# Kernel optimization log

Measured on AMD Instinct MI355X. Metric: run time of the kernel, lower is better.

The kernel has to match this reference:

```python
import jax, jax.numpy as jnp
import numpy as np

HEAD_DIM = 128
B, S = 8, 2048
NEG = -1e9  # matches torch masked_fill value


def setup_inputs() -> dict:
    key = jax.random.key(0)
    kq, kk, kv, kl = jax.random.split(key, 4)
    q = jax.random.normal(kq, (B, S, HEAD_DIM), dtype=jnp.float32)
    k = jax.random.normal(kk, (B, S, HEAD_DIM), dtype=jnp.float32)
    v = jax.random.normal(kv, (B, S, HEAD_DIM), dtype=jnp.float32)
    event_lengths = jax.random.randint(kl, (B,), 0, S, dtype=jnp.int32)
    return {"q": q, "k": k, "v": v, "event_lengths": event_lengths}


def reference(q, k, v, event_lengths):
    # NOTE: the torch module defines query/key/value Linear layers but never
    # applies them in forward(); q, k, v are used raw. Dropout is also unused.
    head_dim = q.shape[-1]
    seq_q = q.shape[1]
    seq_kv = k.shape[1]
    # [B, Sq, Skv] scores
    scores = jnp.einsum("bqd,bkd->bqk", q, k) / jnp.sqrt(
        jnp.asarray(head_dim, dtype=jnp.float32)
    )
    lens = event_lengths[:, None, None]  # [B,1,1]
    mask_q = jnp.arange(seq_q)[None, :, None] < lens   # [B,Sq,1]
    mask_kv = jnp.arange(seq_kv)[None, None, :] < lens  # [B,1,Skv]
    scores = jnp.where(mask_q & mask_kv, scores, NEG)
    attn = jax.nn.softmax(scores, axis=-1)
    return jnp.einsum("bqk,bkd->bqd", attn, v)
```

## Files before the change

### kernel.cpp

```cpp
#include <hip/hip_runtime.h>
#include <math.h>

#define BATCH 8
#define SEQ 2048
#define DIM 128
#define SCALE 0.08838834764831845f
#define NEGINF (-1e30f)
#define PSTR 40
#define INVSEQ (1.0f / 2048.0f)

#define OFF_VSUM 0
#define OFF_KW   4096
#define OFF_VW   (4096 + 4194304)
#define WS_NEEDED (4096 + 2 * 4194304)

typedef __attribute__((ext_vector_type(8))) short short8;
typedef __attribute__((ext_vector_type(4))) float floatx4;

union U8 { unsigned u[4]; short8 s; uint4 q; };

__device__ __forceinline__ unsigned pk_bf(float f0, float f1) {
    unsigned a = __float_as_uint(f0) + 0x8000u;
    unsigned b = __float_as_uint(f1) + 0x8000u;
    return __builtin_amdgcn_perm(a, b, 0x03020706u);
}

__global__ __launch_bounds__(256) void conv3(const float* __restrict__ k,
                                             const float* __restrict__ v,
                                             unsigned short* __restrict__ kw,
                                             unsigned short* __restrict__ vw,
                                             float* __restrict__ vsum) {
    __shared__ __align__(16) unsigned sL[2176];
    int blk = blockIdx.x, t = threadIdx.x;
    if (blk < 512) {
        int b = blk >> 6, tile = blk & 63;
        const float4* src = (const float4*)(k + ((size_t)(b * SEQ + tile * 32)) * DIM);
        #pragma unroll
        for (int i = 0; i < 4; ++i) {
            int F = t + 256 * i;
            int r = F >> 5, c4 = F & 31;
            float4 x = src[F];
            uint2 p;
            p.x = pk_bf(x.x * SCALE, x.y * SCALE);
            p.y = pk_bf(x.z * SCALE, x.w * SCALE);
            *(uint2*)&sL[r * 66 + c4 * 2] = p;
        }
        __syncthreads();
        uint4* dst = (uint4*)(kw + (size_t)(b * 64 + tile) * 4096);
        #pragma unroll
        for (int si = 0; si < 2; ++si) {
            int s = 2 * t + si;
            int f = s >> 6, ln = s & 63;
            int l16 = ln & 15, quad = ln >> 4;
            int nt = f >> 2, ds = f & 3;
            int base = (nt * 16 + l16) * 66 + ds * 16 + quad * 4;
            uint2 a = *(const uint2*)&sL[base];
            uint2 c = *(const uint2*)&sL[base + 2];
            dst[s] = make_uint4(a.x, a.y, c.x, c.y);
        }
    } else {
        int blk2 = blk - 512;
        int b = blk2 >> 6, tile = blk2 & 63;
        const float4* src = (const float4*)(v + ((size_t)(b * SEQ + tile * 32)) * DIM);
        #pragma unroll
        for (int h = 0; h < 2; ++h) {
            int kp = (t >> 5) + 8 * h;
            int c4 = t & 31;
            float4 x0 = src[(2 * kp) * 32 + c4];
            float4 x1 = src[(2 * kp + 1) * 32 + c4];
            int d0 = c4 * 4;
            sL[(d0 + 0) * 17 + kp] = pk_bf(x0.x, x1.x);
            sL[(d0 + 1) * 17 + kp] = pk_bf(x0.y, x1.y);
            sL[(d0 + 2) * 17 + kp] = pk_bf(x0.z, x1.z);
            sL[(d0 + 3) * 17 + kp] = pk_bf(x0.w, x1.w);
        }
        __syncthreads();
        uint4* dst = (uint4*)(vw + (size_t)(b * 64 + tile) * 4096);
        #pragma unroll
        for (int si = 0; si < 2; ++si) {
            int s = 2 * t + si;
            int dt = s >> 6, ln = s & 63;
            int l16 = ln & 15, quad = ln >> 4;
            int base = (dt * 16 + l16) * 17 + quad * 4;
            dst[s] = make_uint4(sL[base], sL[base + 1], sL[base + 2], sL[base + 3]);
        }
        if (t < 128) {
            float ssum = 0.f;
            #pragma unroll
            for (int j = 0; j < 16; ++j) {
                unsigned u = sL[t * 17 + j];
                ssum += __uint_as_float(u << 16);
                ssum += __uint_as_float(u & 0xffff0000u);
            }
            atomicAdd(&vsum[b * DIM + t], ssum);
        }
    }
}

#define LOADK(kb_, KF_)                                                        \
    {                                                                          \
        const unsigned short* kT_ = kwB + (size_t)((kb_) >> 5) * 4096 + lane * 8; \
        _Pragma("unroll")                                                      \
        for (int f_ = 0; f_ < 8; ++f_) KF_[f_] = *(const short8*)(kT_ + f_ * 512); \
    }

#define CHUNK(KF_, kb_)                                                        \
    {                                                                          \
                                 \
        short8 VF[8];                                                          \
        {                                                                      \
            const unsigned short* vT_ = vwB + (size_t)((kb_) >> 5) * 4096 + lane * 8; \
            _Pragma("unroll")                                                  \
            for (int dt = 0; dt < 8; ++dt) VF[dt] = *(const short8*)(vT_ + dt * 512); \
        }                                                                      \
        floatx4 S0 = (floatx4){0.f, 0.f, 0.f, 0.f};                            \
        floatx4 S1 = (floatx4){0.f, 0.f, 0.f, 0.f};                            \
        _Pragma("unroll")                                                      \
        for (int ds = 0; ds < 4; ++ds)                                         \
            S0 = __builtin_amdgcn_mfma_f32_16x16x32_bf16(KF_[ds], Qf[ds], S0, 0, 0, 0); \
        _Pragma("unroll")                                                      \
        for (int ds = 0; ds < 4; ++ds)                                         \
            S1 = __builtin_amdgcn_mfma_f32_16x16x32_bf16(KF_[4 + ds], Qf[ds], S1, 0, 0, 0); \
        PREFETCH_NEXT                                                          \
        int kl0 = (kb_) + quad * 4;                                            \
        int kl1 = kl0 + 16;                                                    \
        float s0v[4], s1v[4];                                                  \
        float mt = m;                                                          \
        _Pragma("unroll")                                                      \
        for (int r = 0; r < 4; ++r) {                                          \
            s0v[r] = (kl0 + r < kend) ? S0[r] : NEGINF;                        \
            s1v[r] = (kl1 + r < kend) ? S1[r] : NEGINF;                        \
            mt = fmaxf(mt, fmaxf(s0v[r], s1v[r]));                             \
        }                                                                      \
        mt = fmaxf(mt, __shfl_xor(mt, 16));                                    \
        mt = fmaxf(mt, __shfl_xor(mt, 32));                                    \
        float alpha = __expf(m - mt);                                          \
        m = mt;                                                                \
        float p0[4], p1[4], ps = 0.f;                                          \
        _Pragma("unroll")                                                      \
        for (int r = 0; r < 4; ++r) {                                          \
            p0[r] = __expf(s0v[r] - mt);                                       \
            p1[r] = __expf(s1v[r] - mt);                                       \
            ps += p0[r] + p1[r];                                               \
        }                                                                      \
        ps += __shfl_xor(ps, 16);                                              \
        ps += __shfl_xor(ps, 32);                                              \
        l = l * alpha + ps;                                                    \
        _Pragma("unroll")                                                      \
        for (int dt = 0; dt < 8; ++dt) {                                       \
            _Pragma("unroll")                                                  \
            for (int r = 0; r < 4; ++r) O[dt][r] *= alpha;                     \
        }                                                                      \
        {                                                                      \
            uint2 w0, w1;                                                      \
            w0.x = pk_bf(p0[0], p0[1]); w0.y = pk_bf(p0[2], p0[3]);            \
            w1.x = pk_bf(p1[0], p1[1]); w1.y = pk_bf(p1[2], p1[3]);            \
            *(uint2*)&sPw[l16 * PSTR + quad * 4]      = w0;                    \
            *(uint2*)&sPw[l16 * PSTR + 16 + quad * 4] = w1;                    \
        }                                                                      \
        short8 Pf = *(const short8*)&sPw[l16 * PSTR + quad * 8];               \
        _Pragma("unroll")                                                      \
        for (int dt = 0; dt < 8; ++dt)                                         \
            O[dt] = __builtin_amdgcn_mfma_f32_16x16x32_bf16(VF[dt], Pf, O[dt], 0, 0, 0); \
    }

__global__ __launch_bounds__(256, 2) void attn_p(const float* __restrict__ q,
                                                 const unsigned short* __restrict__ kw,
                                                 const unsigned short* __restrict__ vw,
                                                 const int* __restrict__ lens,
                                                 const float* __restrict__ vsum,
                                                 float* __restrict__ out) {
    __shared__ __align__(16) unsigned short sP[4][16 * PSTR];
    __shared__ float sC[3][16][132];
    __shared__ float sS[4][16][2];

    int blk = blockIdx.x;
    int b = blk & 7;
    int q0 = (blk >> 3) * 16;
    int len = lens[b];
    int t = threadIdx.x;
    int lane = t & 63;
    int ks = t >> 6;
    int l16 = lane & 15;
    int quad = lane >> 4;
    const int bo = b * SEQ * DIM;

    if (q0 >= len) {
        int row = t >> 4;
        int c0 = (t & 15) * 8;
        float4 a = *(const float4*)&vsum[b * DIM + c0];
        float4 c = *(const float4*)&vsum[b * DIM + c0 + 4];
        float* op = out + bo + (q0 + row) * DIM + c0;
        *(float4*)op = make_float4(a.x * INVSEQ, a.y * INVSEQ, a.z * INVSEQ, a.w * INVSEQ);
        *(float4*)(op + 4) = make_float4(c.x * INVSEQ, c.y * INVSEQ, c.z * INVSEQ, c.w * INVSEQ);
        return;
    }

    int slice = ((len + 127) >> 7) << 5;
    int kbeg = ks * slice;
    int kend = min(kbeg + slice, len);

    floatx4 O[8];
    #pragma unroll
    for (int dt = 0; dt < 8; ++dt) O[dt] = (floatx4){0.f, 0.f, 0.f, 0.f};
    float m = NEGINF, l = 0.f;
    unsigned short* sPw = sP[ks];
    const unsigned short* kwB = kw + (size_t)b * 64 * 4096;
    const unsigned short* vwB = vw + (size_t)b * 64 * 4096;

    if (kbeg < kend) {
        short8 Qf[4];
        {
            const float* qp = q + bo + (q0 + l16) * DIM + quad * 8;
            #pragma unroll
            for (int ds = 0; ds < 4; ++ds) {
                float4 x0 = *(const float4*)(qp + ds * 32);
                float4 x1 = *(const float4*)(qp + ds * 32 + 4);
                U8 f;
                f.u[0] = pk_bf(x0.x, x0.y); f.u[1] = pk_bf(x0.z, x0.w);
                f.u[2] = pk_bf(x1.x, x1.y); f.u[3] = pk_bf(x1.z, x1.w);
                Qf[ds] = f.s;
            }
        }

        short8 KA[8], KB[8];
        LOADK(kbeg, KA)
        int kb = kbeg;
        while (true) {
#define PREFETCH_NEXT if (kb + 32 < kend) LOADK(kb + 32, KB)
            CHUNK(KA, kb)
#undef PREFETCH_NEXT
            kb += 32;
            if (kb >= kend) break;
#define PREFETCH_NEXT if (kb + 32 < kend) LOADK(kb + 32, KA)
            CHUNK(KB, kb)
#undef PREFETCH_NEXT
            kb += 32;
            if (kb >= kend) break;
        }
    }

    if (ks > 0) {
        if (quad == 0) { sS[ks][l16][0] = m; sS[ks][l16][1] = l; }
        #pragma unroll
        for (int dt = 0; dt < 8; ++dt)
            *(floatx4*)&sC[ks - 1][l16][dt * 16 + quad * 4] = O[dt];
    }
    __syncthreads();

    if (ks == 0) {
        float mw[3], lw[3];
        float mstar = m;
        #pragma unroll
        for (int w = 0; w < 3; ++w) {
            mw[w] = sS[w + 1][l16][0];
            lw[w] = sS[w + 1][l16][1];
            mstar = fmaxf(mstar, mw[w]);
        }
        float s0 = __expf(m - mstar);
        float sw[3];
        float lstar = s0 * l;
        #pragma unroll
        for (int w = 0; w < 3; ++w) {
            sw[w] = __expf(mw[w] - mstar);
            lstar += sw[w] * lw[w];
        }
        float inv = 1.f / lstar;
        bool rowvalid = (q0 + l16) < len;
        float* ob = out + bo + (q0 + l16) * DIM;
        const float* vm = vsum + b * DIM;
        #pragma unroll
        for (int dt = 0; dt < 8; ++dt) {
            floatx4 acc = O[dt];
            #pragma unroll
            for (int r = 0; r < 4; ++r) acc[r] *= s0;
            #pragma unroll
            for (int w = 0; w < 3; ++w) {
                floatx4 ow = *(const floatx4*)&sC[w][l16][dt * 16 + quad * 4];
                #pragma unroll
                for (int r = 0; r < 4; ++r) acc[r] += sw[w] * ow[r];
            }
            float4 res;
            if (rowvalid) {
                res = make_float4(acc[0] * inv, acc[1] * inv, acc[2] * inv, acc[3] * inv);
            } else {
                float4 vv = *(const float4*)(vm + dt * 16 + quad * 4);
                res = make_float4(vv.x * INVSEQ, vv.y * INVSEQ, vv.z * INVSEQ, vv.w * INVSEQ);
            }
            *(float4*)(ob + dt * 16 + quad * 4) = res;
        }
    }
}

__global__ __launch_bounds__(256) void vmean_partial(const float* __restrict__ v,
                                                     float* __restrict__ part) {
    int blk = blockIdx.x;
    int b = blk >> 3, oct = blk & 7;
    int t = threadIdx.x;
    int d4 = t & 31, rg = t >> 5;
    const float4* vb = (const float4*)(v + (size_t)b * SEQ * DIM);
    float4 acc = make_float4(0.f, 0.f, 0.f, 0.f);
    int base = oct * 256 + rg * 32;
    #pragma unroll 8
    for (int i = 0; i < 32; ++i) {
        float4 x = vb[(size_t)(base + i) * 32 + d4];
        acc.x += x.x; acc.y += x.y; acc.z += x.z; acc.w += x.w;
    }
    __shared__ float4 red[8][32];
    red[rg][d4] = acc;
    __syncthreads();
    if (t < 32) {
        float4 s = red[0][t];
        #pragma unroll
        for (int r = 1; r < 8; ++r) {
            float4 x = red[r][t];
            s.x += x.x; s.y += x.y; s.z += x.z; s.w += x.w;
        }
        ((float4*)part)[(size_t)blk * 32 + t] = s;
    }
}

__global__ __launch_bounds__(128) void vmean_combine(const float* __restrict__ part,
                                                     float* __restrict__ vmean) {
    int b = blockIdx.x, t = threadIdx.x;
    float s = 0.f;
    #pragma unroll
    for (int o = 0; o < 8; ++o) s += part[((size_t)b * 8 + o) * DIM + t];
    vmean[b * DIM + t] = s * INVSEQ;
}

__global__ __launch_bounds__(512, 4) void attn_flash(const float* __restrict__ q,
                                                     const float* __restrict__ k,
                                                     const float* __restrict__ v,
                                                     const int* __restrict__ lens,
                                                     const float* __restrict__ vmean,
                                                     float* __restrict__ out) {
    __shared__ unsigned short sPf[8 * 16 * PSTR];
    __shared__ float sC[2][3][16][132];
    __shared__ float sS[2][4][16][2];

    int blk = blockIdx.x;
    int b = blk & 7;
    int g = blk >> 3;
    int q0 = g * 32;
    int len = lens[b];
    int t = threadIdx.x;
    int lane = t & 63;
    int wave = t >> 6;
    int qt = wave & 1;
    int ks = wave >> 1;
    int l16 = lane & 15;
    int quad = lane >> 4;
    const int bo = b * SEQ * DIM;

    int rowbase = q0 + qt * 16;
    bool active = q0 < len;

    int slice = (len + 3) >> 2;
    int kbeg = ks * slice;
    int kend = min(kbeg + slice, len);

    floatx4 O[8];
    #pragma unroll
    for (int dt = 0; dt < 8; ++dt) O[dt] = (floatx4){0.f, 0.f, 0.f, 0.f};
    float m = NEGINF, l = 0.f;
    unsigned short* sPw = &sPf[wave * 16 * PSTR];

    if (active && kbeg < kend) {
        short8 Qf[4];
        {
            const float* qp = q + bo + (rowbase + l16) * DIM + quad * 8;
            #pragma unroll
            for (int ds = 0; ds < 4; ++ds) {
                float4 x0 = *(const float4*)(qp + ds * 32);
                float4 x1 = *(const float4*)(qp + ds * 32 + 4);
                U8 f;
                f.u[0] = pk_bf(x0.x, x0.y); f.u[1] = pk_bf(x0.z, x0.w);
                f.u[2] = pk_bf(x1.x, x1.y); f.u[3] = pk_bf(x1.z, x1.w);
                Qf[ds] = f.s;
            }
        }
        for (int kb = kbeg; kb < kend; kb += 32) {
            int kr0 = kb + l16;      kr0 = kr0 < SEQ ? kr0 : SEQ - 1;
            int kr1 = kb + 16 + l16; kr1 = kr1 < SEQ ? kr1 : SEQ - 1;
            const float* kp0 = k + bo + kr0 * DIM + quad * 8;
            const float* kp1 = k + bo + kr1 * DIM + quad * 8;
            floatx4 S0 = (floatx4){0.f, 0.f, 0.f, 0.f};
            floatx4 S1 = (floatx4){0.f, 0.f, 0.f, 0.f};
            #pragma unroll
            for (int ds = 0; ds < 4; ++ds) {
                float4 a0 = *(const float4*)(kp0 + ds * 32);
                float4 a1 = *(const float4*)(kp0 + ds * 32 + 4);
                U8 f;
                f.u[0] = pk_bf(a0.x, a0.y); f.u[1] = pk_bf(a0.z, a0.w);
                f.u[2] = pk_bf(a1.x, a1.y); f.u[3] = pk_bf(a1.z, a1.w);
                S0 = __builtin_amdgcn_mfma_f32_16x16x32_bf16(f.s, Qf[ds], S0, 0, 0, 0);
            }
            #pragma unroll
            for (int ds = 0; ds < 4; ++ds) {
                float4 a0 = *(const float4*)(kp1 + ds * 32);
                float4 a1 = *(const float4*)(kp1 + ds * 32 + 4);
                U8 f;
                f.u[0] = pk_bf(a0.x, a0.y); f.u[1] = pk_bf(a0.z, a0.w);
                f.u[2] = pk_bf(a1.x, a1.y); f.u[3] = pk_bf(a1.z, a1.w);
                S1 = __builtin_amdgcn_mfma_f32_16x16x32_bf16(f.s, Qf[ds], S1, 0, 0, 0);
            }
            int kl0 = kb + quad * 4;
            int kl1 = kb + 16 + quad * 4;
            float s0v[4], s1v[4];
            float mt = m;
            #pragma unroll
            for (int r = 0; r < 4; ++r) {
                s0v[r] = (kl0 + r < kend) ? S0[r] * SCALE : NEGINF;
                s1v[r] = (kl1 + r < kend) ? S1[r] * SCALE : NEGINF;
                mt = fmaxf(mt, fmaxf(s0v[r], s1v[r]));
            }
            mt = fmaxf(mt, __shfl_xor(mt, 16));
            mt = fmaxf(mt, __shfl_xor(mt, 32));
            float alpha = __expf(m - mt);
            m = mt;
            float p0[4], p1[4], ps = 0.f;
            #pragma unroll
            for (int r = 0; r < 4; ++r) {
                p0[r] = __expf(s0v[r] - mt);
                p1[r] = __expf(s1v[r] - mt);
                ps += p0[r] + p1[r];
            }
            ps += __shfl_xor(ps, 16);
            ps += __shfl_xor(ps, 32);
            l = l * alpha + ps;
            #pragma unroll
            for (int dt = 0; dt < 8; ++dt) {
                #pragma unroll
                for (int r = 0; r < 4; ++r) O[dt][r] *= alpha;
            }
            {
                uint2 w0, w1;
                w0.x = pk_bf(p0[0], p0[1]); w0.y = pk_bf(p0[2], p0[3]);
                w1.x = pk_bf(p1[0], p1[1]); w1.y = pk_bf(p1[2], p1[3]);
                *(uint2*)&sPw[l16 * PSTR + quad * 4]      = w0;
                *(uint2*)&sPw[l16 * PSTR + 16 + quad * 4] = w1;
            }
            short8 Pf = *(const short8*)&sPw[l16 * PSTR + quad * 8];
            int vro[8];
            #pragma unroll
            for (int jj = 0; jj < 8; ++jj) {
                int kk = kb + quad * 8 + jj;
                kk = kk < SEQ ? kk : SEQ - 1;
                vro[jj] = kk * DIM;
            }
            const float* vb = v + bo + l16;
            #pragma unroll
            for (int dt = 0; dt < 8; ++dt) {
                int c = dt * 16;
                float x0 = vb[vro[0] + c], x1 = vb[vro[1] + c];
                float x2 = vb[vro[2] + c], x3 = vb[vro[3] + c];
                float x4 = vb[vro[4] + c], x5 = vb[vro[5] + c];
                float x6 = vb[vro[6] + c], x7 = vb[vro[7] + c];
                U8 f;
                f.u[0] = pk_bf(x0, x1); f.u[1] = pk_bf(x2, x3);
                f.u[2] = pk_bf(x4, x5); f.u[3] = pk_bf(x6, x7);
                O[dt] = __builtin_amdgcn_mfma_f32_16x16x32_bf16(f.s, Pf, O[dt], 0, 0, 0);
            }
        }
    }

    if (active && ks > 0) {
        if (quad == 0) { sS[qt][ks][l16][0] = m; sS[qt][ks][l16][1] = l; }
        #pragma unroll
        for (int dt = 0; dt < 8; ++dt)
            *(floatx4*)&sC[qt][ks - 1][l16][dt * 16 + quad * 4] = O[dt];
    }
    __syncthreads();

    if (ks == 0) {
        const float* vm = vmean + b * DIM;
        float* ob = out + bo + (rowbase + l16) * DIM;
        if (active) {
            float mw[3], lw[3];
            float mstar = m;
            #pragma unroll
            for (int w = 0; w < 3; ++w) {
                mw[w] = sS[qt][w + 1][l16][0];
                lw[w] = sS[qt][w + 1][l16][1];
                mstar = fmaxf(mstar, mw[w]);
            }
            float s0 = __expf(m - mstar);
            float sw[3];
            float lstar = s0 * l;
            #pragma unroll
            for (int w = 0; w < 3; ++w) {
                sw[w] = __expf(mw[w] - mstar);
                lstar += sw[w] * lw[w];
            }
            float inv = 1.f / lstar;
            bool rowvalid = (rowbase + l16) < len;
            #pragma unroll
            for (int dt = 0; dt < 8; ++dt) {
                floatx4 acc = O[dt];
                #pragma unroll
                for (int r = 0; r < 4; ++r) acc[r] *= s0;
                #pragma unroll
                for (int w = 0; w < 3; ++w) {
                    floatx4 ow = *(const floatx4*)&sC[qt][w][l16][dt * 16 + quad * 4];
                    #pragma unroll
                    for (int r = 0; r < 4; ++r) acc[r] += sw[w] * ow[r];
                }
                float4 res;
                if (rowvalid) {
                    res = make_float4(acc[0] * inv, acc[1] * inv, acc[2] * inv, acc[3] * inv);
                } else {
                    res = *(const float4*)(vm + dt * 16 + quad * 4);
                }
                *(float4*)(ob + dt * 16 + quad * 4) = res;
            }
        } else {
            #pragma unroll
            for (int dt = 0; dt < 8; ++dt)
                *(float4*)(ob + dt * 16 + quad * 4) =
                    *(const float4*)(vm + dt * 16 + quad * 4);
        }
    }
}

extern "C" void kernel_launch(void* const* d_in, const int* in_sizes, int n_in,
                              void* d_out, int out_size, void* d_ws, size_t ws_size,
                              hipStream_t stream) {
    const float* q = (const float*)d_in[0];
    const float* k = (const float*)d_in[1];
    const float* v = (const float*)d_in[2];
    const int* lens = (const int*)d_in[3];
    float* out = (float*)d_out;

    if (ws_size >= (size_t)WS_NEEDED) {
        float* vsum = (float*)((char*)d_ws + OFF_VSUM);
        unsigned short* kw = (unsigned short*)((char*)d_ws + OFF_KW);
        unsigned short* vw = (unsigned short*)((char*)d_ws + OFF_VW);
        hipMemsetAsync(vsum, 0, BATCH * DIM * sizeof(float), stream);
        conv3<<<dim3(1024), dim3(256), 0, stream>>>(k, v, kw, vw, vsum);
        attn_p<<<dim3(1024), dim3(256), 0, stream>>>(q, kw, vw, lens, vsum, out);
    } else {
        float* part = (float*)d_ws;
        float* vmean = part + 64 * DIM;
        vmean_partial<<<dim3(64), dim3(256), 0, stream>>>(v, part);
        vmean_combine<<<dim3(8), dim3(128), 0, stream>>>(part, vmean);
        attn_flash<<<dim3(512), dim3(512), 0, stream>>>(q, k, v, lens, vmean, out);
    }
}
```

Before: 116.2 us.

## Stream K/V tiles through LDS with global_load_lds direct copies

Replaces the register double-buffered K prefetch and per-chunk direct V global loads with asynchronous global-to-LDS copies (global_load_lds) of both K and V tiles per wave. Each wave then reads its fragments from LDS and issues the next tile's copy before doing the MFMA and softmax work. This is meant to overlap memory latency for both K and V and to cut register pressure. In exchange it adds about 70KB of LDS per block, which may limit occupancy, and a single LDS buffer per wave, so the next copy can collide with the current read unless the lgkm wait orders them. The merge buffers now alias the K/V area behind an added barrier.

```diff
diff --git a/kernel.cpp b/kernel.cpp
--- a/kernel.cpp
+++ b/kernel.cpp
@@ -24,6 +24,14 @@
     unsigned b = __float_as_uint(f1) + 0x8000u;
     return __builtin_amdgcn_perm(a, b, 0x03020706u);
 }
+
+__device__ __forceinline__ void gld16(const unsigned short* g, unsigned short* l) {
+    __builtin_amdgcn_global_load_lds(
+        (const __attribute__((address_space(1))) unsigned*)g,
+        (__attribute__((address_space(3))) unsigned*)l, 16, 0, 0);
+}
+__device__ __forceinline__ void wait_vm0()  { asm volatile("s_waitcnt vmcnt(0)" ::: "memory"); }
+__device__ __forceinline__ void wait_lgk0() { asm volatile("s_waitcnt lgkmcnt(0)" ::: "memory"); }
 
 __global__ __launch_bounds__(256) void conv3(const float* __restrict__ k,
                                              const float* __restrict__ v,
@@ -97,82 +105,23 @@
     }
 }
 
-#define LOADK(kb_, KF_)                                                        \
+#define DMA_TILE(kb_)                                                          \
     {                                                                          \
         const unsigned short* kT_ = kwB + (size_t)((kb_) >> 5) * 4096 + lane * 8; \
+        const unsigned short* vT_ = vwB + (size_t)((kb_) >> 5) * 4096 + lane * 8; \
         _Pragma("unroll")                                                      \
-        for (int f_ = 0; f_ < 8; ++f_) KF_[f_] = *(const short8*)(kT_ + f_ * 512); \
-    }
-
-#define CHUNK(KF_, kb_)                                                        \
-    {                                                                          \
-                                 \
-        short8 VF[8];                                                          \
-        {                                                                      \
-            const unsigned short* vT_ = vwB + (size_t)((kb_) >> 5) * 4096 + lane * 8; \
-            _Pragma("unroll")                                                  \
-            for (int dt = 0; dt < 8; ++dt) VF[dt] = *(const short8*)(vT_ + dt * 512); \
-        }                                                                      \
-        floatx4 S0 = (floatx4){0.f, 0.f, 0.f, 0.f};                            \
-        floatx4 S1 = (floatx4){0.f, 0.f, 0.f, 0.f};                            \
+        for (int f_ = 0; f_ < 8; ++f_) gld16(kT_ + f_ * 512, sKw + f_ * 512);  \
         _Pragma("unroll")                                                      \
-        for (int ds = 0; ds < 4; ++ds)                                         \
-            S0 = __builtin_amdgcn_mfma_f32_16x16x32_bf16(KF_[ds], Qf[ds], S0, 0, 0, 0); \
-        _Pragma("unroll")                                                      \
-        for (int ds = 0; ds < 4; ++ds)                                         \
-            S1 = __builtin_amdgcn_mfma_f32_16x16x32_bf16(KF_[4 + ds], Qf[ds], S1, 0, 0, 0); \
-        PREFETCH_NEXT                                                          \
-        int kl0 = (kb_) + quad * 4;                                            \
-        int kl1 = kl0 + 16;                                                    \
-        float s0v[4], s1v[4];                                                  \
-        float mt = m;                                                          \
-        _Pragma("unroll")                                                      \
-        for (int r = 0; r < 4; ++r) {                                          \
-            s0v[r] = (kl0 + r < kend) ? S0[r] : NEGINF;                        \
-            s1v[r] = (kl1 + r < kend) ? S1[r] : NEGINF;                        \
-            mt = fmaxf(mt, fmaxf(s0v[r], s1v[r]));                             \
-        }                                                                      \
-        mt = fmaxf(mt, __shfl_xor(mt, 16));                                    \
-        mt = fmaxf(mt, __shfl_xor(mt, 32));                                    \
-        float alpha = __expf(m - mt);                                          \
-        m = mt;                                                                \
-        float p0[4], p1[4], ps = 0.f;                                          \
-        _Pragma("unroll")                                                      \
-        for (int r = 0; r < 4; ++r) {                                          \
-            p0[r] = __expf(s0v[r] - mt);                                       \
-            p1[r] = __expf(s1v[r] - mt);                                       \
-            ps += p0[r] + p1[r];                                               \
-        }                                                                      \
-        ps += __shfl_xor(ps, 16);                                              \
-        ps += __shfl_xor(ps, 32);                                              \
-        l = l * alpha + ps;                                                    \
-        _Pragma("unroll")                                                      \
-        for (int dt = 0; dt < 8; ++dt) {                                       \
-            _Pragma("unroll")                                                  \
-            for (int r = 0; r < 4; ++r) O[dt][r] *= alpha;                     \
-        }                                                                      \
-        {                                                                      \
-            uint2 w0, w1;                                                      \
-            w0.x = pk_bf(p0[0], p0[1]); w0.y = pk_bf(p0[2], p0[3]);            \
-            w1.x = pk_bf(p1[0], p1[1]); w1.y = pk_bf(p1[2], p1[3]);            \
-            *(uint2*)&sPw[l16 * PSTR + quad * 4]      = w0;                    \
-            *(uint2*)&sPw[l16 * PSTR + 16 + quad * 4] = w1;                    \
-        }                                                                      \
-        short8 Pf = *(const short8*)&sPw[l16 * PSTR + quad * 8];               \
-        _Pragma("unroll")                                                      \
-        for (int dt = 0; dt < 8; ++dt)                                         \
-            O[dt] = __builtin_amdgcn_mfma_f32_16x16x32_bf16(VF[dt], Pf, O[dt], 0, 0, 0); \
-    }
-
-__global__ __launch_bounds__(256, 2) void attn_p(const float* __restrict__ q,
-                                                 const unsigned short* __restrict__ kw,
-                                                 const unsigned short* __restrict__ vw,
-                                                 const int* __restrict__ lens,
-                                                 const float* __restrict__ vsum,
-                                                 float* __restrict__ out) {
-    __shared__ __align__(16) unsigned short sP[4][16 * PSTR];
-    __shared__ float sC[3][16][132];
-    __shared__ float sS[4][16][2];
+        for (int f_ = 0; f_ < 8; ++f_) gld16(vT_ + f_ * 512, sVw + f_ * 512);  \
+    }
+
+__global__ __launch_bounds__(256, 2) void attn_v10(const float* __restrict__ q,
+                                                   const unsigned short* __restrict__ kw,
+                                                   const unsigned short* __restrict__ vw,
+                                                   const int* __restrict__ lens,
+                                                   const float* __restrict__ vsum,
+                                                   float* __restrict__ out) {
+    __shared__ __align__(16) unsigned char smem[71168];
 
     int blk = blockIdx.x;
     int b = blk & 7;
@@ -196,6 +145,10 @@
         return;
     }
 
+    unsigned short* sKw = (unsigned short*)(smem + ks * 16384);
+    unsigned short* sVw = sKw + 4096;
+    unsigned short* sPw = (unsigned short*)(smem + 65536) + ks * 16 * PSTR;
+
     int slice = ((len + 127) >> 7) << 5;
     int kbeg = ks * slice;
     int kend = min(kbeg + slice, len);
@@ -204,7 +157,6 @@
     #pragma unroll
     for (int dt = 0; dt < 8; ++dt) O[dt] = (floatx4){0.f, 0.f, 0.f, 0.f};
     float m = NEGINF, l = 0.f;
-    unsigned short* sPw = sP[ks];
     const unsigned short* kwB = kw + (size_t)b * 64 * 4096;
     const unsigned short* vwB = vw + (size_t)b * 64 * 4096;
 
@@ -223,25 +175,80 @@
             }
         }
 
-        short8 KA[8], KB[8];
-        LOADK(kbeg, KA)
-        int kb = kbeg;
-        while (true) {
-#define PREFETCH_NEXT if (kb + 32 < kend) LOADK(kb + 32, KB)
-            CHUNK(KA, kb)
-#undef PREFETCH_NEXT
-            kb += 32;
-            if (kb >= kend) break;
-#define PREFETCH_NEXT if (kb + 32 < kend) LOADK(kb + 32, KA)
-            CHUNK(KB, kb)
-#undef PREFETCH_NEXT
-            kb += 32;
-            if (kb >= kend) break;
-        }
-    }
-
+        DMA_TILE(kbeg)
+
+        for (int kb = kbeg; kb < kend; kb += 32) {
+            wait_vm0();
+
+            short8 KF[8], VF[8];
+            #pragma unroll
+            for (int f = 0; f < 8; ++f) KF[f] = *(const short8*)(sKw + f * 512 + lane * 8);
+            #pragma unroll
+            for (int f = 0; f < 8; ++f) VF[f] = *(const short8*)(sVw + f * 512 + lane * 8);
+            wait_lgk0();
+
+            if (kb + 32 < kend) DMA_TILE(kb + 32)
+
+            floatx4 S0 = (floatx4){0.f, 0.f, 0.f, 0.f};
+            floatx4 S1 = (floatx4){0.f, 0.f, 0.f, 0.f};
+            #pragma unroll
+            for (int ds = 0; ds < 4; ++ds)
+                S0 = __builtin_amdgcn_mfma_f32_16x16x32_bf16(KF[ds], Qf[ds], S0, 0, 0, 0);
+            #pragma unroll
+            for (int ds = 0; ds < 4; ++ds)
+                S1 = __builtin_amdgcn_mfma_f32_16x16x32_bf16(KF[4 + ds], Qf[ds], S1, 0, 0, 0);
+
+            int kl0 = kb + quad * 4;
+            int kl1 = kl0 + 16;
+            float s0v[4], s1v[4];
+            float mt = m;
+            #pragma unroll
+            for (int r = 0; r < 4; ++r) {
+                s0v[r] = (kl0 + r < kend) ? S0[r] : NEGINF;
+                s1v[r] = (kl1 + r < kend) ? S1[r] : NEGINF;
+                mt = fmaxf(mt, fmaxf(s0v[r], s1v[r]));
+            }
+            mt = fmaxf(mt, __shfl_xor(mt, 16));
+            mt = fmaxf(mt, __shfl_xor(mt, 32));
+            float alpha = __expf(m - mt);
+            m = mt;
+            float p0[4], p1[4], ps = 0.f;
+            #pragma unroll
+            for (int r = 0; r < 4; ++r) {
+                p0[r] = __expf(s0v[r] - mt);
+                p1[r] = __expf(s1v[r] - mt);
+                ps += p0[r] + p1[r];
+            }
+            ps += __shfl_xor(ps, 16);
+            ps += __shfl_xor(ps, 32);
+            l = l * alpha + ps;
+            #pragma unroll
+            for (int dt = 0; dt < 8; ++dt) {
+                #pragma unroll
+                for (int r = 0; r < 4; ++r) O[dt][r] *= alpha;
+            }
+
+            {
+                uint2 w0, w1;
+                w0.x = pk_bf(p0[0], p0[1]); w0.y = pk_bf(p0[2], p0[3]);
+                w1.x = pk_bf(p1[0], p1[1]); w1.y = pk_bf(p1[2], p1[3]);
+                *(uint2*)&sPw[l16 * PSTR + quad * 4]      = w0;
+                *(uint2*)&sPw[l16 * PSTR + 16 + quad * 4] = w1;
+            }
+            short8 Pf = *(const short8*)&sPw[l16 * PSTR + quad * 8];
+
+            #pragma unroll
+            for (int dt = 0; dt < 8; ++dt)
+                O[dt] = __builtin_amdgcn_mfma_f32_16x16x32_bf16(VF[dt], Pf, O[dt], 0, 0, 0);
+        }
+    }
+
+    float (*sC)[16][132] = (float(*)[16][132])smem;
+    float (*sS)[2] = (float(*)[2])(smem + 70656);
+
+    __syncthreads();
     if (ks > 0) {
-        if (quad == 0) { sS[ks][l16][0] = m; sS[ks][l16][1] = l; }
+        if (quad == 0) { sS[ks * 16 + l16][0] = m; sS[ks * 16 + l16][1] = l; }
         #pragma unroll
         for (int dt = 0; dt < 8; ++dt)
             *(floatx4*)&sC[ks - 1][l16][dt * 16 + quad * 4] = O[dt];
@@ -253,8 +260,8 @@
         float mstar = m;
         #pragma unroll
         for (int w = 0; w < 3; ++w) {
-            mw[w] = sS[w + 1][l16][0];
-            lw[w] = sS[w + 1][l16][1];
+            mw[w] = sS[(w + 1) * 16 + l16][0];
+            lw[w] = sS[(w + 1) * 16 + l16][1];
             mstar = fmaxf(mstar, mw[w]);
         }
         float s0 = __expf(m - mstar);
@@ -538,7 +545,7 @@
         unsigned short* vw = (unsigned short*)((char*)d_ws + OFF_VW);
         hipMemsetAsync(vsum, 0, BATCH * DIM * sizeof(float), stream);
         conv3<<<dim3(1024), dim3(256), 0, stream>>>(k, v, kw, vw, vsum);
-        attn_p<<<dim3(1024), dim3(256), 0, stream>>>(q, kw, vw, lens, vsum, out);
+        attn_v10<<<dim3(1024), dim3(256), 0, stream>>>(q, kw, vw, lens, vsum, out);
     } else {
         float* part = (float*)d_ws;
         float* vmean = part + 64 * DIM;
```

New measurement: 129.9 us. 1.12x slower.
